# Optimization experiments

Hardware: AMD Instinct MI355X
Metric: run time of the kernel (lower is better)

The kernel has to match this reference:

```python
import jax, jax.numpy as jnp
import numpy as np


def _set_abstraction(xyz, points, npoint, nsample, w1, b1, w2, b2, w3, b3):
    """xyz: (B,3,N), points: (B,C,N) or None. Returns (new_xyz, new_points).
    BN (eval mode) is folded into conv weights/biases; conv1x1 == einsum over channels.
    Deterministic sampling: take first `npoint` points (stand-in for randperm)."""
    B, _, N = xyz.shape
    if npoint is None:
        new_xyz = xyz
        P = N
    else:
        new_xyz = xyz[:, :, :npoint]
        P = npoint
    # squared pairwise distances (B,P,N); topk indices match cdist topk (sqrt monotone)
    xs = jnp.sum(new_xyz * new_xyz, axis=1)            # (B,P)
    ys = jnp.sum(xyz * xyz, axis=1)                    # (B,N)
    d2 = xs[:, :, None] + ys[:, None, :] - 2.0 * jnp.einsum('bcp,bcn->bpn', new_xyz, xyz)
    _, idx = jax.lax.top_k(-d2, nsample)               # (B,P,K) nearest neighbors
    idx4 = idx[:, None, :, :]                          # (B,1,P,K)
    grouped_xyz = jnp.take_along_axis(xyz[:, :, None, :], idx4, axis=3)  # (B,3,P,K)
    grouped_xyz = grouped_xyz - new_xyz[:, :, :, None]
    if points is not None:
        grouped_pts = jnp.take_along_axis(points[:, :, None, :], idx4, axis=3)  # (B,C,P,K)
        feat = jnp.concatenate([grouped_xyz, grouped_pts], axis=1)
    else:
        feat = grouped_xyz
    h = jax.nn.relu(jnp.einsum('oc,bcpk->bopk', w1, feat) + b1[None, :, None, None])
    h = jax.nn.relu(jnp.einsum('oc,bcpk->bopk', w2, h) + b2[None, :, None, None])
    h = jnp.einsum('oc,bcpk->bopk', w3, h) + b3[None, :, None, None]  # no relu before max
    new_points = jnp.max(h, axis=3)                    # (B,C_out,P) max over nsample
    return new_xyz, new_points


def setup_inputs() -> dict:
    key = jax.random.key(0)
    ks = iter(jax.random.split(key, 32))
    B, N, C_IN, NUM_CLASSES = 32, 4096, 6, 40

    def w(k, co, ci):
        return jax.random.normal(k, (co, ci), dtype=jnp.float32) * (1.0 / np.sqrt(ci))

    def b(k, co):
        return jax.random.normal(k, (co,), dtype=jnp.float32) * 0.01

    inp = {'x': jax.random.normal(next(ks), (B, C_IN, N), dtype=jnp.float32)}
    # sa1: in = 3 feat + 3 rel-xyz = 6
    inp['sa1_w1'] = w(next(ks), 64, 6);    inp['sa1_b1'] = b(next(ks), 64)
    inp['sa1_w2'] = w(next(ks), 64, 64);   inp['sa1_b2'] = b(next(ks), 64)
    inp['sa1_w3'] = w(next(ks), 128, 64);  inp['sa1_b3'] = b(next(ks), 128)
    # sa2: in = 128 + 3 = 131
    inp['sa2_w1'] = w(next(ks), 128, 131); inp['sa2_b1'] = b(next(ks), 128)
    inp['sa2_w2'] = w(next(ks), 128, 128); inp['sa2_b2'] = b(next(ks), 128)
    inp['sa2_w3'] = w(next(ks), 256, 128); inp['sa2_b3'] = b(next(ks), 256)
    # sa3: in = 256 + 3 = 259
    inp['sa3_w1'] = w(next(ks), 256, 259); inp['sa3_b1'] = b(next(ks), 256)
    inp['sa3_w2'] = w(next(ks), 512, 256); inp['sa3_b2'] = b(next(ks), 512)
    inp['sa3_w3'] = w(next(ks), 1024, 512); inp['sa3_b3'] = b(next(ks), 1024)
    # fc head (BN folded, dropout in eval mode = identity)
    inp['fc1_w'] = w(next(ks), 512, 1024); inp['fc1_b'] = b(next(ks), 512)
    inp['fc2_w'] = w(next(ks), 256, 512);  inp['fc2_b'] = b(next(ks), 256)
    inp['fc3_w'] = w(next(ks), NUM_CLASSES, 256); inp['fc3_b'] = b(next(ks), NUM_CLASSES)
    return inp


def reference(x, sa1_w1, sa1_b1, sa1_w2, sa1_b2, sa1_w3, sa1_b3,
              sa2_w1, sa2_b1, sa2_w2, sa2_b2, sa2_w3, sa2_b3,
              sa3_w1, sa3_b1, sa3_w2, sa3_b2, sa3_w3, sa3_b3,
              fc1_w, fc1_b, fc2_w, fc2_b, fc3_w, fc3_b):
    xyz = x[:, :3, :]
    pts = x[:, 3:, :]
    xyz1, p1 = _set_abstraction(xyz, pts, 512, 32, sa1_w1, sa1_b1, sa1_w2, sa1_b2, sa1_w3, sa1_b3)
    xyz2, p2 = _set_abstraction(xyz1, p1, 128, 64, sa2_w1, sa2_b1, sa2_w2, sa2_b2, sa2_w3, sa2_b3)
    _, p3 = _set_abstraction(xyz2, p2, None, 1, sa3_w1, sa3_b1, sa3_w2, sa3_b2, sa3_w3, sa3_b3)
    g = jnp.max(p3, axis=2)                               # (B,1024) global max pool
    h = jax.nn.relu(g @ fc1_w.T + fc1_b)                  # dropout eval = identity
    h = jax.nn.relu(h @ fc2_w.T + fc2_b)
    return h @ fc3_w.T + fc3_b                            # (B,num_classes)
```

## Files before the change

kernel.cpp:

```cpp
#include <hip/hip_runtime.h>
#include <hip/hip_bf16.h>

#define FLT_BIG 3.0e38f

typedef __attribute__((ext_vector_type(8))) short s8v;
typedef __attribute__((ext_vector_type(4))) float f4v;

__device__ inline void split2(float v, unsigned short& h0, unsigned short& h1) {
    unsigned int u = __float_as_uint(v);
    unsigned int r0 = (u + 0x7FFFu + ((u >> 16) & 1u)) >> 16;
    h0 = (unsigned short)r0;
    float r = v - __uint_as_float(r0 << 16);
    unsigned int u2 = __float_as_uint(r);
    h1 = (unsigned short)((u2 + 0x7FFFu + ((u2 >> 16) & 1u)) >> 16);
}

#define SA2_P1(AI, BI)                                                          \
    _Pragma("unroll") for (int oi = 0; oi < 2; oi++) {                          \
        _Pragma("unroll") for (int jf = 0; jf < 4; jf++)                        \
            acc1[oi][jf] = __builtin_amdgcn_mfma_f32_16x16x32_bf16(             \
                aw[oi][AI], bfr[jf][BI], acc1[oi][jf], 0, 0, 0);                \
    }
#define SA1_P1(AI, BI)                                                          \
    _Pragma("unroll") for (int jf = 0; jf < 4; jf++)                            \
        acc1[jf] = __builtin_amdgcn_mfma_f32_16x16x32_bf16(                     \
            aw[AI], bfr[jf][BI], acc1[jf], 0, 0, 0);
#define MM_P2(AI, BI)                                                           \
    _Pragma("unroll") for (int oi = 0; oi < 2; oi++) {                          \
        _Pragma("unroll") for (int jf = 0; jf < 4; jf++)                        \
            acc2[oi][jf] = __builtin_amdgcn_mfma_f32_16x16x32_bf16(             \
                af[jf][AI], gw[oi][BI], acc2[oi][jf], 0, 0, 0);                 \
    }
#define SA3_P(AI, BI)                                                           \
    _Pragma("unroll") for (int oi = 0; oi < 2; oi++) {                          \
        _Pragma("unroll") for (int j = 0; j < 4; j++)                           \
            acc[oi][ph * 4 + j] = __builtin_amdgcn_mfma_f32_16x16x32_bf16(      \
                aw[oi][AI], bfh[j][BI], acc[oi][ph * 4 + j], 0, 0, 0);          \
    }

#define MKKEY(QX, QY, QZ, XS)                                                   \
    ({  float dot_ = fmaf((QZ), yz, fmaf((QY), yy, (QX) * yx));                 \
        float d2_ = fmaf(-2.0f, dot_, (XS) + ys);                               \
        unsigned int kk_ = __float_as_uint(d2_);                                \
        (kk_ & 0x80000000u) ? ~kk_ : (kk_ | 0x80000000u); })

struct WfragJob { const float* W; int K, stride, off, no; unsigned short* out; };
struct WfragJobs { WfragJob j[4]; int start[5]; };

__global__ __launch_bounds__(64) void wfrag_multi(WfragJobs jobs) {
    int bid = blockIdx.x;
    int ji = 3;
    if (bid < jobs.start[1]) ji = 0;
    else if (bid < jobs.start[2]) ji = 1;
    else if (bid < jobs.start[3]) ji = 2;
    const WfragJob& J = jobs.j[ji];
    int lb = bid - jobs.start[ji];
    int l = threadIdx.x;
    int ks = lb / J.no, ot = lb - ks * J.no;
    int o = ot * 16 + (l & 15);
    int k0 = ks * 32 + (l >> 4) * 8;
    const float* src = J.W + (size_t)o * J.stride + J.off + k0;
    unsigned short h[2][8];
#pragma unroll
    for (int e = 0; e < 8; e++) split2(src[e], h[0][e], h[1][e]);
#pragma unroll
    for (int p = 0; p < 2; p++) {
        s8v v;
#pragma unroll
        for (int e = 0; e < 8; e++) v[e] = (short)h[p][e];
        *(s8v*)(J.out + ((size_t)(lb * 2 + p) * 64 + l) * 8) = v;
    }
}

#define KNN_CAP 192
__global__ __launch_bounds__(256) void knn4_kernel(
    const float* __restrict__ x, int N_pts, int K, int P,
    int* __restrict__ idx_out, unsigned short* __restrict__ idx16) {
    int bq = blockIdx.x;
    int pg = P >> 2;
    int b = bq / pg, p0 = (bq - b * pg) * 4;
    const float* xyz = x + (size_t)b * 24576;
    __shared__ unsigned int hist[2][2048];
    __shared__ unsigned int candK[4][KNN_CAP];
    __shared__ int candI[4][KNN_CAP];
    __shared__ int outIdx[4][64];
    __shared__ unsigned int cnts[4][2];
    __shared__ int sB[4], sM[4];
    __shared__ float qcoord[4][4];
    int t = threadIdx.x;
    int w = t >> 6, lane = t & 63;
    for (int i = t; i < 4096; i += 256) ((unsigned int*)hist)[i] = 0u;
    if (t < 8) cnts[t >> 1][t & 1] = 0u;
    float qx[4], qy[4], qz[4], xs[4];
#pragma unroll
    for (int q = 0; q < 4; q++) {
        float a = xyz[p0 + q], c1 = xyz[4096 + p0 + q], c2 = xyz[8192 + p0 + q];
        qx[q] = a; qy[q] = c1; qz[q] = c2;
        xs[q] = fmaf(c2, c2, fmaf(c1, c1, a * a));
    }
    if (t < 4) {
        qcoord[t][0] = qx[t]; qcoord[t][1] = qy[t];
        qcoord[t][2] = qz[t]; qcoord[t][3] = xs[t];
    }
    __syncthreads();
    for (int n = t; n < N_pts; n += 256) {
        float yx = xyz[n], yy = xyz[4096 + n], yz = xyz[8192 + n];
        float ys = fmaf(yz, yz, fmaf(yy, yy, yx * yx));
#pragma unroll
        for (int q = 0; q < 4; q++) {
            unsigned int key = MKKEY(qx[q], qy[q], qz[q], xs[q]);
            atomicAdd(&hist[q >> 1][key >> 21], 1u << ((q & 1) * 16));
        }
    }
    __syncthreads();
    {
        int pair = w >> 1, sh = (w & 1) * 16;
        unsigned int lsum = 0;
        for (int i = 0; i < 32; i++)
            lsum += (hist[pair][lane * 32 + i] >> sh) & 0xFFFFu;
        unsigned int incl = lsum;
        for (int ss = 1; ss < 64; ss <<= 1) {
            unsigned int v = (unsigned int)__shfl_up((int)incl, ss);
            if (lane >= ss) incl += v;
        }
        unsigned int excl = incl - lsum;
        if (excl < (unsigned)K && excl + lsum >= (unsigned)K) {
            unsigned int cum = excl;
            for (int i = 0; i < 32; i++) {
                unsigned int h = (hist[pair][lane * 32 + i] >> sh) & 0xFFFFu;
                if (cum < (unsigned)K && cum + h >= (unsigned)K) {
                    sB[w] = lane * 32 + i; sM[w] = (int)cum; break;
                }
                cum += h;
            }
        }
    }
    __syncthreads();
    for (int n = t; n < N_pts; n += 256) {
        float yx = xyz[n], yy = xyz[4096 + n], yz = xyz[8192 + n];
        float ys = fmaf(yz, yz, fmaf(yy, yy, yx * yx));
#pragma unroll
        for (int q = 0; q < 4; q++) {
            unsigned int key = MKKEY(qx[q], qy[q], qz[q], xs[q]);
            int bin = (int)(key >> 21);
            int Bq = sB[q];
            if (bin < Bq) {
                outIdx[q][atomicAdd(&cnts[q][0], 1u)] = n;
            } else if (bin == Bq) {
                unsigned int ci = atomicAdd(&cnts[q][1], 1u);
                if (ci < KNN_CAP) { candK[q][ci] = key; candI[q][ci] = n; }
            }
        }
    }
    __syncthreads();
    {
        int nc = (int)cnts[w][1];
        int m = sM[w], r = K - m, Bw = sB[w];
        if (nc <= KNN_CAP) {
            for (int ci = lane; ci < nc; ci += 64) {
                unsigned int ki = candK[w][ci];
                int ii = candI[w][ci];
                int rank = 0;
                for (int j = 0; j < nc; j++) {
                    unsigned int kj = candK[w][j];
                    rank += (kj < ki || (kj == ki && candI[w][j] < ii)) ? 1 : 0;
                }
                if (rank < r) outIdx[w][m + rank] = ii;
            }
        } else {
            float fqx = qcoord[w][0], fqy = qcoord[w][1];
            float fqz = qcoord[w][2], fxs = qcoord[w][3];
            unsigned int lastK = 0u; int lastI = -1;
            for (int rr = 0; rr < r; rr++) {
                unsigned int bk = 0xFFFFFFFFu; int bi = 0x7fffffff;
                for (int n = lane; n < N_pts; n += 64) {
                    float yx = xyz[n], yy = xyz[4096 + n], yz = xyz[8192 + n];
                    float ys = fmaf(yz, yz, fmaf(yy, yy, yx * yx));
                    unsigned int key = MKKEY(fqx, fqy, fqz, fxs);
                    if ((int)(key >> 21) == Bw) {
                        bool gt = (key > lastK) || (key == lastK && n > lastI);
                        if (gt && (key < bk || (key == bk && n < bi))) { bk = key; bi = n; }
                    }
                }
#pragma unroll
                for (int ss = 32; ss > 0; ss >>= 1) {
                    unsigned int ok = (unsigned int)__shfl_xor((int)bk, ss);
                    int oi = __shfl_xor(bi, ss);
                    if (ok < bk || (ok == bk && oi < bi)) { bk = ok; bi = oi; }
                }
                if (lane == 0) outIdx[w][m + rr] = bi;
                lastK = bk; lastI = bi;
            }
        }
    }
    __syncthreads();
    if (t < 4 * K) {
        int q = t / K, k = t - q * K;
        size_t off = ((size_t)(b * P) + p0 + q) * K + k;
        if (idx16) idx16[off] = (unsigned short)outIdx[q][k];
        else idx_out[off] = outIdx[q][k];
    }
}

__global__ __launch_bounds__(256) void sa1_pre_kernel(
    const float* __restrict__ x, const float* __restrict__ w1, const float* __restrict__ b1,
    float* __restrict__ a1t) {
    int bid = blockIdx.x;
    int b = bid >> 5, nt = bid & 31, n0 = nt << 7;
    __shared__ float xsh[6 * 128];
    __shared__ float wt[6 * 68];
    const float* xb = x + (size_t)b * 24576;
    int t = threadIdx.x;
    for (int id = t; id < 768; id += 256) {
        int c = id >> 7, n = id & 127;
        xsh[c * 128 + n] = xb[c * 4096 + n0 + n];
    }
    for (int id = t; id < 384; id += 256) {
        int c = id >> 6, o = id & 63;
        wt[c * 68 + o] = w1[o * 6 + c];
    }
    __syncthreads();
    int o = t & 63, ng = t >> 6;
    float acc[32];
    float bias = b1[o];
#pragma unroll
    for (int j = 0; j < 32; j++) acc[j] = bias;
    for (int c = 0; c < 6; c++) {
        float w = wt[c * 68 + o];
        const float* f = &xsh[c * 128 + ng * 32];
#pragma unroll
        for (int j = 0; j < 32; j++) acc[j] += w * f[j];
    }
#pragma unroll
    for (int j = 0; j < 32; j++)
        a1t[((size_t)b * 4096 + n0 + ng * 32 + j) * 64 + o] = acc[j];
}

__global__ __launch_bounds__(256) void sa1_mfma_kernel(
    const float* __restrict__ x, const float* __restrict__ a1t,
    const int* __restrict__ idx1, const float* __restrict__ w1,
    const unsigned short* __restrict__ w2f, const float* __restrict__ b2,
    const unsigned short* __restrict__ w3f, const float* __restrict__ b3,
    float* __restrict__ p1) {
    int bp = blockIdx.x;
    int b = bp >> 8, pp = bp & 255, p0 = pp * 2;
    __shared__ float dshq[2][64];
    __shared__ int nbr[64];
    __shared__ unsigned short A1buf[8 * 2 * 64 * 8];
    __shared__ float MX[2][128];
    const float* xb = x + (size_t)b * 24576;
    int t = threadIdx.x;
    int w = t >> 6, l = t & 63;
    int n16 = l & 15, og = l >> 4;
    if (t < 64) nbr[t] = idx1[((size_t)b * 512 + p0) * 32 + t];
    if (t < 128) {
        int qi = t >> 6, c = t & 63;
        float qx = xb[p0 + qi], qy = xb[4096 + p0 + qi], qz = xb[8192 + p0 + qi];
        dshq[qi][c] = -(w1[c * 6 + 0] * qx + w1[c * 6 + 1] * qy + w1[c * 6 + 2] * qz);
    }
    __syncthreads();
    int q = w >> 1;
    f4v acc1[4];
#pragma unroll
    for (int jf = 0; jf < 4; jf++) acc1[jf] = (f4v){0.f, 0.f, 0.f, 0.f};
    const float* gsrc = a1t + ((size_t)b * 4096 + nbr[w * 16 + n16]) * 64 + og * 8;
    f4v nv0 = *(const f4v*)(gsrc);
    f4v nv1 = *(const f4v*)(gsrc + 4);
    s8v nw[2];
    {
        const s8v* wr = (const s8v*)w2f;
#pragma unroll
        for (int pl = 0; pl < 2; pl++) nw[pl] = wr[(w * 2 + pl) * 64 + l];
    }
    for (int ks = 0; ks < 2; ks++) {
        f4v v0 = nv0, v1 = nv1;
        s8v aw[2];
#pragma unroll
        for (int pl = 0; pl < 2; pl++) aw[pl] = nw[pl];
        if (ks < 1) {
            nv0 = *(const f4v*)(gsrc + 32);
            nv1 = *(const f4v*)(gsrc + 36);
            const s8v* wr = (const s8v*)w2f + (size_t)4 * 2 * 64;
#pragma unroll
            for (int pl = 0; pl < 2; pl++) nw[pl] = wr[(w * 2 + pl) * 64 + l];
        }
        unsigned short* BFD = A1buf + (ks & 1) * 4096;
        const float* d = &dshq[q][ks * 32 + og * 8];
        s8v sp0, sp1;
#pragma unroll
        for (int e = 0; e < 8; e++) {
            float hv = fmaxf(((e < 4) ? v0[e] : v1[e - 4]) + d[e], 0.f);
            unsigned short h0, h1;
            split2(hv, h0, h1);
            sp0[e] = (short)h0; sp1[e] = (short)h1;
        }
        *(s8v*)&BFD[((w * 2 + 0) * 64 + l) * 8] = sp0;
        *(s8v*)&BFD[((w * 2 + 1) * 64 + l) * 8] = sp1;
        __syncthreads();
        s8v bfr[4][2];
#pragma unroll
        for (int jf = 0; jf < 4; jf++)
#pragma unroll
            for (int pl = 0; pl < 2; pl++)
                bfr[jf][pl] = *(const s8v*)&BFD[((jf * 2 + pl) * 64 + l) * 8];
        SA1_P1(1, 0) SA1_P1(0, 1) SA1_P1(0, 0)
    }
    __syncthreads();
    {
        f4v bv = *(const f4v*)(b2 + w * 16 + og * 4);
        int l2 = n16 + ((w & 1) * 2 + (og >> 1)) * 16;
        int half = og & 1;
#pragma unroll
        for (int jf = 0; jf < 4; jf++) {
            unsigned short hh[2][4];
#pragma unroll
            for (int r = 0; r < 4; r++) {
                float y = fmaxf(acc1[jf][r] + bv[r], 0.f);
                split2(y, hh[0][r], hh[1][r]);
            }
            int slot = (w >> 1) * 4 + jf;
#pragma unroll
            for (int pl = 0; pl < 2; pl++) {
                unsigned long long pk = (unsigned long long)hh[pl][0] |
                    ((unsigned long long)hh[pl][1] << 16) |
                    ((unsigned long long)hh[pl][2] << 32) |
                    ((unsigned long long)hh[pl][3] << 48);
                *(unsigned long long*)&A1buf[((slot * 2 + pl) * 64 + l2) * 8 + half * 4] = pk;
            }
        }
    }
    __syncthreads();
    f4v acc2[2][4];
#pragma unroll
    for (int oi = 0; oi < 2; oi++)
#pragma unroll
        for (int jf = 0; jf < 4; jf++) acc2[oi][jf] = (f4v){0.f, 0.f, 0.f, 0.f};
    for (int ks2 = 0; ks2 < 2; ks2++) {
        s8v af[4][2];
#pragma unroll
        for (int jf = 0; jf < 4; jf++)
#pragma unroll
            for (int pl = 0; pl < 2; pl++)
                af[jf][pl] = *(const s8v*)&A1buf[(((ks2 * 4 + jf) * 2 + pl) * 64 + l) * 8];
        const s8v* wr = (const s8v*)w3f + (size_t)(ks2 * 8) * 2 * 64;
        s8v gw[2][2];
#pragma unroll
        for (int oi = 0; oi < 2; oi++)
#pragma unroll
            for (int pl = 0; pl < 2; pl++)
                gw[oi][pl] = wr[((w * 2 + oi) * 2 + pl) * 64 + l];
        MM_P2(1, 0) MM_P2(0, 1) MM_P2(0, 0)
    }
#pragma unroll
    for (int oi = 0; oi < 2; oi++) {
        float m0 = fmaxf(fmaxf(acc2[oi][0][0], acc2[oi][0][1]),
                         fmaxf(acc2[oi][0][2], acc2[oi][0][3]));
        m0 = fmaxf(m0, fmaxf(fmaxf(acc2[oi][1][0], acc2[oi][1][1]),
                             fmaxf(acc2[oi][1][2], acc2[oi][1][3])));
        float m1 = fmaxf(fmaxf(acc2[oi][2][0], acc2[oi][2][1]),
                         fmaxf(acc2[oi][2][2], acc2[oi][2][3]));
        m1 = fmaxf(m1, fmaxf(fmaxf(acc2[oi][3][0], acc2[oi][3][1]),
                             fmaxf(acc2[oi][3][2], acc2[oi][3][3])));
        m0 = fmaxf(m0, __shfl_xor(m0, 16));
        m0 = fmaxf(m0, __shfl_xor(m0, 32));
        m1 = fmaxf(m1, __shfl_xor(m1, 16));
        m1 = fmaxf(m1, __shfl_xor(m1, 32));
        if (og == 0) {
            MX[0][(w * 2 + oi) * 16 + n16] = m0;
            MX[1][(w * 2 + oi) * 16 + n16] = m1;
        }
    }
    __syncthreads();
    {
        int o = t & 127, qq = t >> 7;
        p1[((size_t)b * 128 + o) * 512 + p0 + qq] = MX[qq][o] + b3[o];
    }
}

__global__ __launch_bounds__(256) void sa2_pre_kernel(
    const float* __restrict__ x, const float* __restrict__ p1,
    const float* __restrict__ w1, const float* __restrict__ b1,
    float* __restrict__ a2t) {
    int bid = blockIdx.x;
    int b = bid >> 2, nt = bid & 3, n0 = nt << 7;
    __shared__ float ins[2][16 * 128];
    __shared__ float wt[2][16 * 132];
    const float* xb = x + (size_t)b * 24576;
    const float* p1b = p1 + (size_t)b * 65536;
    int t = threadIdx.x;
    int og = t >> 3, pg = t & 7;
    int o0 = og * 4;
    float acc[4][16];
    {
        float bl[4] = {b1[o0], b1[o0 + 1], b1[o0 + 2], b1[o0 + 3]};
#pragma unroll
        for (int oi = 0; oi < 4; oi++)
#pragma unroll
            for (int j = 0; j < 16; j++) acc[oi][j] = bl[oi];
    }
    for (int id = t; id < 16 * 128; id += 256) {
        int n = id & 127, c = id >> 7;
        ins[0][c * 128 + n] = (c < 3) ? xb[c * 4096 + n0 + n]
                                      : p1b[(size_t)(c - 3) * 512 + n0 + n];
    }
    for (int id = t; id < 2048; id += 256) {
        int c = id & 15, oo = id >> 4;
        wt[0][c * 132 + oo] = w1[oo * 131 + c];
    }
    __syncthreads();
    for (int ch = 0; ch < 9; ch++) {
        int cs = (ch == 8) ? 3 : 16;
        if (ch < 8) {
            int c0n = (ch + 1) * 16;
            int csn = (ch == 7) ? 3 : 16;
            int nb = (ch + 1) & 1;
            for (int id = t; id < csn * 128; id += 256) {
                int n = id & 127, c = id >> 7;
                int cg = c0n + c;
                ins[nb][c * 128 + n] = (cg < 3) ? xb[cg * 4096 + n0 + n]
                                                : p1b[(size_t)(cg - 3) * 512 + n0 + n];
            }
            for (int id = t; id < 2048; id += 256) {
                int c = id & 15, oo = id >> 4;
                if (c < csn) wt[nb][c * 132 + oo] = w1[oo * 131 + c0n + c];
            }
        }
        const float* wb = wt[ch & 1];
        const float* ib = ins[ch & 1];
        for (int cc = 0; cc < cs; cc++) {
            float4 wv = *(const float4*)&wb[cc * 132 + o0];
            float wl[4] = {wv.x, wv.y, wv.z, wv.w};
#pragma unroll
            for (int c4 = 0; c4 < 4; c4++) {
                float4 fv = *(const float4*)&ib[cc * 128 + pg * 4 + c4 * 32];
                float fl[4] = {fv.x, fv.y, fv.z, fv.w};
#pragma unroll
                for (int j = 0; j < 4; j++)
#pragma unroll
                    for (int oi = 0; oi < 4; oi++) acc[oi][c4 * 4 + j] += wl[oi] * fl[j];
            }
        }
        __syncthreads();
    }
#pragma unroll
    for (int c4 = 0; c4 < 4; c4++)
#pragma unroll
        for (int j = 0; j < 4; j++) {
            int n = n0 + pg * 4 + c4 * 32 + j;
            float4 v;
            v.x = acc[0][c4 * 4 + j]; v.y = acc[1][c4 * 4 + j];
            v.z = acc[2][c4 * 4 + j]; v.w = acc[3][c4 * 4 + j];
            *(float4*)&a2t[((size_t)b * 512 + n) * 128 + o0] = v;
        }
}

__global__ __launch_bounds__(256) void sa2_mfma_kernel(
    const float* __restrict__ x, const float* __restrict__ a2t,
    const unsigned short* __restrict__ idx2, const float* __restrict__ w1,
    const unsigned short* __restrict__ w2f, const float* __restrict__ b2,
    const unsigned short* __restrict__ w3f, const float* __restrict__ b3,
    unsigned short* __restrict__ p2f) {
    int bp = blockIdx.x;
    int b = bp >> 7, p = bp & 127;
    __shared__ float dsh[128];
    __shared__ int nbr[64];
    __shared__ unsigned short A2buf[16 * 2 * 64 * 8];
    __shared__ float MX[256];
    const float* xb = x + (size_t)b * 24576;
    int t = threadIdx.x;
    int w = t >> 6, l = t & 63;
    int n16 = l & 15, og = l >> 4;
    if (t < 64) nbr[t] = (int)idx2[((size_t)b * 128 + p) * 64 + t];
    if (t < 128) {
        float qx = xb[p], qy = xb[4096 + p], qz = xb[8192 + p];
        dsh[t] = -(w1[t * 131 + 0] * qx + w1[t * 131 + 1] * qy + w1[t * 131 + 2] * qz);
    }
    __syncthreads();
    f4v acc1[2][4];
#pragma unroll
    for (int oi = 0; oi < 2; oi++)
#pragma unroll
        for (int jf = 0; jf < 4; jf++) acc1[oi][jf] = (f4v){0.f, 0.f, 0.f, 0.f};
    const float* gsrc = a2t + ((size_t)b * 512 + nbr[w * 16 + n16]) * 128 + og * 8;
    f4v nv0 = *(const f4v*)(gsrc);
    f4v nv1 = *(const f4v*)(gsrc + 4);
    s8v nw[2][2];
    {
        const s8v* wr = (const s8v*)w2f;
#pragma unroll
        for (int oi = 0; oi < 2; oi++)
#pragma unroll
            for (int pl = 0; pl < 2; pl++)
                nw[oi][pl] = wr[((w * 2 + oi) * 2 + pl) * 64 + l];
    }
    for (int ks = 0; ks < 4; ks++) {
        f4v v0 = nv0, v1 = nv1;
        s8v aw[2][2];
#pragma unroll
        for (int oi = 0; oi < 2; oi++)
#pragma unroll
            for (int pl = 0; pl < 2; pl++) aw[oi][pl] = nw[oi][pl];
        if (ks < 3) {
            nv0 = *(const f4v*)(gsrc + (ks + 1) * 32);
            nv1 = *(const f4v*)(gsrc + (ks + 1) * 32 + 4);
            const s8v* wr = (const s8v*)w2f + (size_t)((ks + 1) * 8) * 2 * 64;
#pragma unroll
            for (int oi = 0; oi < 2; oi++)
#pragma unroll
                for (int pl = 0; pl < 2; pl++)
                    nw[oi][pl] = wr[((w * 2 + oi) * 2 + pl) * 64 + l];
        }
        unsigned short* BFD = A2buf + (ks & 1) * 4096;
        const float* d = &dsh[ks * 32 + og * 8];
        s8v sp0, sp1;
#pragma unroll
        for (int e = 0; e < 8; e++) {
            float hv = fmaxf(((e < 4) ? v0[e] : v1[e - 4]) + d[e], 0.f);
            unsigned short h0, h1;
            split2(hv, h0, h1);
            sp0[e] = (short)h0; sp1[e] = (short)h1;
        }
        *(s8v*)&BFD[((w * 2 + 0) * 64 + l) * 8] = sp0;
        *(s8v*)&BFD[((w * 2 + 1) * 64 + l) * 8] = sp1;
        __syncthreads();
        s8v bfr[4][2];
#pragma unroll
        for (int jf = 0; jf < 4; jf++)
#pragma unroll
            for (int pl = 0; pl < 2; pl++)
                bfr[jf][pl] = *(const s8v*)&BFD[((jf * 2 + pl) * 64 + l) * 8];
        SA2_P1(1, 0) SA2_P1(0, 1) SA2_P1(0, 0)
    }
    __syncthreads();
#pragma unroll
    for (int oi = 0; oi < 2; oi++) {
        int ot = w * 2 + oi;
        f4v bv = *(const f4v*)(b2 + ot * 16 + og * 4);
        int l2 = n16 + (oi * 2 + (og >> 1)) * 16;
        int half = og & 1;
#pragma unroll
        for (int jf = 0; jf < 4; jf++) {
            unsigned short hh[2][4];
#pragma unroll
            for (int r = 0; r < 4; r++) {
                float y = fmaxf(acc1[oi][jf][r] + bv[r], 0.f);
                split2(y, hh[0][r], hh[1][r]);
            }
            int slot = w * 4 + jf;
#pragma unroll
            for (int pl = 0; pl < 2; pl++) {
                unsigned long long pk = (unsigned long long)hh[pl][0] |
                    ((unsigned long long)hh[pl][1] << 16) |
                    ((unsigned long long)hh[pl][2] << 32) |
                    ((unsigned long long)hh[pl][3] << 48);
                *(unsigned long long*)&A2buf[((slot * 2 + pl) * 64 + l2) * 8 + half * 4] = pk;
            }
        }
    }
    __syncthreads();
#pragma unroll
    for (int half2 = 0; half2 < 2; half2++) {
        f4v acc2[2][4];
#pragma unroll
        for (int oi = 0; oi < 2; oi++)
#pragma unroll
            for (int jf = 0; jf < 4; jf++) acc2[oi][jf] = (f4v){0.f, 0.f, 0.f, 0.f};
        for (int ks2 = 0; ks2 < 4; ks2++) {
            s8v af[4][2];
#pragma unroll
            for (int jf = 0; jf < 4; jf++)
#pragma unroll
                for (int pl = 0; pl < 2; pl++)
                    af[jf][pl] = *(const s8v*)&A2buf[(((ks2 * 4 + jf) * 2 + pl) * 64 + l) * 8];
            const s8v* wr = (const s8v*)w3f + (size_t)(ks2 * 16) * 2 * 64;
            s8v gw[2][2];
#pragma unroll
            for (int oi = 0; oi < 2; oi++)
#pragma unroll
                for (int pl = 0; pl < 2; pl++)
                    gw[oi][pl] = wr[((w * 4 + half2 * 2 + oi) * 2 + pl) * 64 + l];
            MM_P2(1, 0) MM_P2(0, 1) MM_P2(0, 0)
        }
#pragma unroll
        for (int oi = 0; oi < 2; oi++) {
            float m = -FLT_BIG;
#pragma unroll
            for (int jf = 0; jf < 4; jf++) {
                float mj = fmaxf(fmaxf(acc2[oi][jf][0], acc2[oi][jf][1]),
                                 fmaxf(acc2[oi][jf][2], acc2[oi][jf][3]));
                m = fmaxf(m, mj);
            }
            m = fmaxf(m, __shfl_xor(m, 16));
            m = fmaxf(m, __shfl_xor(m, 32));
            if (og == 0) MX[(w * 4 + half2 * 2 + oi) * 16 + n16] = m;
        }
    }
    __syncthreads();
    {
        float val = MX[t] + b3[t];
        unsigned short h0, h1;
        split2(val, h0, h1);
        int pt = p >> 4;
        int ks = t >> 5, kl = t & 31;
        int l2 = (p & 15) + (kl >> 3) * 16;
        int e = kl & 7;
        size_t fb = (((size_t)b * 64 + ks * 8 + pt) * 2) * 512 + l2 * 8 + e;
        p2f[fb] = h0;
        p2f[fb + 512] = h1;
    }
}

__global__ __launch_bounds__(64) void sa3_mfma_kernel(
    const unsigned short* __restrict__ hf_in, const unsigned short* __restrict__ wf,
    const float* __restrict__ bias, int nks, int noCout,
    unsigned short* __restrict__ hf_out, int nksOut,
    float* __restrict__ gout, int reduce) {
    int nb = noCout >> 1;
    int bid = blockIdx.x;
    int b = bid / nb, u = bid - b * nb;
    int ot0 = u * 2;
    int l = threadIdx.x;
    f4v acc[2][8];
#pragma unroll
    for (int oi = 0; oi < 2; oi++)
#pragma unroll
        for (int j = 0; j < 8; j++) acc[oi][j] = (f4v){0.f, 0.f, 0.f, 0.f};
    const unsigned short* hb = hf_in + (size_t)b * nks * 8 * 2 * 512;
    for (int ks = 0; ks < nks; ks++) {
        s8v aw[2][2];
#pragma unroll
        for (int oi = 0; oi < 2; oi++)
#pragma unroll
            for (int pl = 0; pl < 2; pl++)
                aw[oi][pl] = *(const s8v*)&wf[(((size_t)(ks * noCout + ot0 + oi)) * 2 + pl) * 512 + l * 8];
#pragma unroll
        for (int ph = 0; ph < 2; ph++) {
            s8v bfh[4][2];
#pragma unroll
            for (int j = 0; j < 4; j++)
#pragma unroll
                for (int pl = 0; pl < 2; pl++)
                    bfh[j][pl] = *(const s8v*)&hb[(((size_t)(ks * 8 + ph * 4 + j)) * 2 + pl) * 512 + l * 8];
            SA3_P(1, 0) SA3_P(0, 1) SA3_P(0, 0)
        }
    }
    if (!reduce) {
#pragma unroll
        for (int oi = 0; oi < 2; oi++) {
            int OT = ot0 + oi;
            f4v bv = *(const f4v*)(bias + OT * 16 + (l >> 4) * 4);
            int ksp = OT >> 1;
            int l2 = (l & 15) + ((OT & 1) * 2 + ((l >> 4) >> 1)) * 16;
            int base4 = ((l >> 4) & 1) * 4;
#pragma unroll
            for (int pt = 0; pt < 8; pt++) {
                unsigned short hh[2][4];
#pragma unroll
                for (int r = 0; r < 4; r++) {
                    float y = fmaxf(acc[oi][pt][r] + bv[r], 0.f);
                    split2(y, hh[0][r], hh[1][r]);
                }
#pragma unroll
                for (int pl = 0; pl < 2; pl++) {
                    unsigned long long pk = (unsigned long long)hh[pl][0] |
                        ((unsigned long long)hh[pl][1] << 16) |
                        ((unsigned long long)hh[pl][2] << 32) |
                        ((unsigned long long)hh[pl][3] << 48);
                    *(unsigned long long*)&hf_out[
                        (((size_t)b * nksOut * 8 + ksp * 8 + pt) * 2 + pl) * 512 + l2 * 8 + base4] = pk;
                }
            }
        }
    } else {
        int Cout = noCout * 16;
#pragma unroll
        for (int oi = 0; oi < 2; oi++) {
            int OT = ot0 + oi;
#pragma unroll
            for (int r = 0; r < 4; r++) {
                float m = acc[oi][0][r];
#pragma unroll
                for (int pt = 1; pt < 8; pt++) m = fmaxf(m, acc[oi][pt][r]);
                m = fmaxf(m, __shfl_xor(m, 1));
                m = fmaxf(m, __shfl_xor(m, 2));
                m = fmaxf(m, __shfl_xor(m, 4));
                m = fmaxf(m, __shfl_xor(m, 8));
                if ((l & 15) == 0) {
                    int o = OT * 16 + ((l >> 4) << 2) + r;
                    gout[(size_t)b * Cout + o] = m + bias[o];
                }
            }
        }
    }
}

__global__ __launch_bounds__(256) void head1_kernel(
    const float* __restrict__ g, const float* __restrict__ fw1,
    const float* __restrict__ fb1, float* __restrict__ h1out) {
    int bid = blockIdx.x;
    int b = bid >> 3, u = bid & 7;
    int o0 = u * 64;
    __shared__ float gs[1024];
    int t = threadIdx.x;
    for (int i = t; i < 1024; i += 256) gs[i] = g[(size_t)b * 1024 + i];
    __syncthreads();
    int o = o0 + (t >> 2), seg = t & 3;
    const float4* wr = (const float4*)&fw1[(size_t)o * 1024 + seg * 256];
    const float* gg0 = &gs[seg * 256];
    float acc = 0.f;
    for (int c = 0; c < 64; c++) {
        float4 wv = wr[c];
        const float* gg = &gg0[c * 4];
        acc += wv.x * gg[0] + wv.y * gg[1] + wv.z * gg[2] + wv.w * gg[3];
    }
    acc += __shfl_down(acc, 1);
    acc += __shfl_down(acc, 2);
    if (seg == 0) h1out[(size_t)b * 512 + o] = fmaxf(acc + fb1[o], 0.f);
}

__global__ __launch_bounds__(256) void head2_kernel(
    const float* __restrict__ h1in,
    const float* __restrict__ fw2, const float* __restrict__ fb2,
    const float* __restrict__ fw3, const float* __restrict__ fb3,
    float* __restrict__ out) {
    int b = blockIdx.x;
    int t = threadIdx.x;
    __shared__ float h1[512];
    __shared__ float h2[256];
    for (int i = t; i < 512; i += 256) h1[i] = h1in[(size_t)b * 512 + i];
    __syncthreads();
    {
        float acc = fb2[t];
        const float4* wr = (const float4*)&fw2[(size_t)t * 512];
        for (int c = 0; c < 128; c++) {
            float4 wv = wr[c];
            acc += wv.x * h1[c * 4] + wv.y * h1[c * 4 + 1] + wv.z * h1[c * 4 + 2] + wv.w * h1[c * 4 + 3];
        }
        h2[t] = fmaxf(acc, 0.f);
    }
    __syncthreads();
    if (t < 40) {
        float acc = fb3[t];
        const float4* wr = (const float4*)&fw3[(size_t)t * 256];
        for (int c = 0; c < 64; c++) {
            float4 wv = wr[c];
            acc += wv.x * h2[c * 4] + wv.y * h2[c * 4 + 1] + wv.z * h2[c * 4 + 2] + wv.w * h2[c * 4 + 3];
        }
        out[b * 40 + t] = acc;
    }
}

extern "C" void kernel_launch(void* const* d_in, const int* in_sizes, int n_in,
                              void* d_out, int out_size, void* d_ws, size_t ws_size,
                              hipStream_t stream) {
    const float* x      = (const float*)d_in[0];
    const float* sa1_w1 = (const float*)d_in[1];
    const float* sa1_b1 = (const float*)d_in[2];
    const float* sa1_w2 = (const float*)d_in[3];
    const float* sa1_b2 = (const float*)d_in[4];
    const float* sa1_w3 = (const float*)d_in[5];
    const float* sa1_b3 = (const float*)d_in[6];
    const float* sa2_w1 = (const float*)d_in[7];
    const float* sa2_b1 = (const float*)d_in[8];
    const float* sa2_w2 = (const float*)d_in[9];
    const float* sa2_b2 = (const float*)d_in[10];
    const float* sa2_w3 = (const float*)d_in[11];
    const float* sa2_b3 = (const float*)d_in[12];
    const float* sa3_w1 = (const float*)d_in[13];
    const float* sa3_b1 = (const float*)d_in[14];
    const float* sa3_w2 = (const float*)d_in[15];
    const float* sa3_b2 = (const float*)d_in[16];
    const float* sa3_w3 = (const float*)d_in[17];
    const float* sa3_b3 = (const float*)d_in[18];
    const float* fc1_w  = (const float*)d_in[19];
    const float* fc1_b  = (const float*)d_in[20];
    const float* fc2_w  = (const float*)d_in[21];
    const float* fc2_b  = (const float*)d_in[22];
    const float* fc3_w  = (const float*)d_in[23];
    const float* fc3_b  = (const float*)d_in[24];

    char* ws = (char*)d_ws;
    const size_t MB = 1048576;
    const size_t KB = 1024;
    unsigned short* s1w2f = (unsigned short*)(ws + 0);
    unsigned short* s1w3f = (unsigned short*)(ws + 32 * KB);
    unsigned short* s2w2f = (unsigned short*)(ws + 128 * KB);
    unsigned short* s2w3f = (unsigned short*)(ws + 224 * KB);
    int*            idx1  = (int*)(ws + 512 * KB);
    unsigned short* idx2  = (unsigned short*)(ws + 2560 * KB);
    float*          a1t   = (float*)(ws + 3 * MB);
    float*          p1    = (float*)(ws + 35 * MB);
    float*          a2t   = (float*)(ws + 4 * MB);
    unsigned short* p2f   = (unsigned short*)(ws + 12 * MB);
    unsigned short* h1f   = (unsigned short*)(ws + 18 * MB);
    unsigned short* h2f   = (unsigned short*)(ws + 24 * MB);
    float*          g     = (float*)(ws + 36 * MB);
    float*          h1hd  = (float*)(ws + 36 * MB + 128 * KB);
    unsigned short* w1f3  = (unsigned short*)(ws + 36 * MB + 512 * KB);
    unsigned short* w2f3  = (unsigned short*)(ws + 37 * MB);
    unsigned short* w3f3  = (unsigned short*)(ws + 38 * MB);

    {
        WfragJobs jobs;
        jobs.j[0] = {sa1_w2, 64, 64, 0, 4, s1w2f};
        jobs.j[1] = {sa1_w3, 64, 64, 0, 8, s1w3f};
        jobs.j[2] = {sa2_w2, 128, 128, 0, 8, s2w2f};
        jobs.j[3] = {sa2_w3, 128, 128, 0, 16, s2w3f};
        jobs.start[0] = 0; jobs.start[1] = 8; jobs.start[2] = 24;
        jobs.start[3] = 56; jobs.start[4] = 120;
        wfrag_multi<<<120, 64, 0, stream>>>(jobs);
    }
    knn4_kernel<<<32 * 128, 256, 0, stream>>>(x, 4096, 32, 512, idx1, nullptr);
    sa1_pre_kernel<<<32 * 32, 256, 0, stream>>>(x, sa1_w1, sa1_b1, a1t);
    sa1_mfma_kernel<<<32 * 256, 256, 0, stream>>>(x, a1t, idx1, sa1_w1,
                                                  s1w2f, sa1_b2, s1w3f, sa1_b3, p1);
    knn4_kernel<<<32 * 32, 256, 0, stream>>>(x, 512, 64, 128, nullptr, idx2);
    sa2_pre_kernel<<<32 * 4, 256, 0, stream>>>(x, p1, sa2_w1, sa2_b1, a2t);
    {
        WfragJobs jobs;
        jobs.j[0] = {sa3_w1, 256, 259, 3, 16, w1f3};
        jobs.j[1] = {sa3_w2, 256, 256, 0, 32, w2f3};
        jobs.j[2] = {sa3_w3, 512, 512, 0, 64, w3f3};
        jobs.j[3] = {sa3_w3, 512, 512, 0, 64, w3f3};
        jobs.start[0] = 0; jobs.start[1] = 128; jobs.start[2] = 384;
        jobs.start[3] = 1408; jobs.start[4] = 1408;
        wfrag_multi<<<1408, 64, 0, stream>>>(jobs);
    }
    sa2_mfma_kernel<<<32 * 128, 256, 0, stream>>>(x, a2t, idx2, sa2_w1,
                                                  s2w2f, sa2_b2, s2w3f, sa2_b3, p2f);
    sa3_mfma_kernel<<<32 * 8, 64, 0, stream>>>(p2f, w1f3, sa3_b1, 8, 16, h1f, 8, nullptr, 0);
    sa3_mfma_kernel<<<32 * 16, 64, 0, stream>>>(h1f, w2f3, sa3_b2, 8, 32, h2f, 16, nullptr, 0);
    sa3_mfma_kernel<<<32 * 32, 64, 0, stream>>>(h2f, w3f3, sa3_b3, 16, 64, nullptr, 0, g, 1);
    head1_kernel<<<32 * 8, 256, 0, stream>>>(g, fc1_w, fc1_b, h1hd);
    head2_kernel<<<32, 256, 0, stream>>>(h1hd, fc2_w, fc2_b, fc3_w, fc3_b,
                                         (float*)d_out);
}
```

Baseline: 397.4 us.

## Cache 16-bit distance keys in LDS and process two queries per KNN block

The KNN kernel now handles two query points per block instead of four, doubling the grid. It stores the top 16 bits of each point's key for both queries in shared memory during the histogram pass. The second pass then reads those cached keys instead of reloading coordinates and recomputing distances. Only candidates in the boundary bin recompute the full key, and the candidate capacity rises to 256. In exchange, half the waves in each block sit idle during the selection phases, and per-block LDS use grows.

After: 425.7 us. +7.1%, slower.

```diff
diff --git a/kernel.cpp b/kernel.cpp
--- a/kernel.cpp
+++ b/kernel.cpp
@@ -72,33 +72,34 @@
     }
 }
 
-#define KNN_CAP 192
-__global__ __launch_bounds__(256) void knn4_kernel(
+#define KNN_CAP 256
+__global__ __launch_bounds__(256) void knn2q_kernel(
     const float* __restrict__ x, int N_pts, int K, int P,
     int* __restrict__ idx_out, unsigned short* __restrict__ idx16) {
     int bq = blockIdx.x;
-    int pg = P >> 2;
-    int b = bq / pg, p0 = (bq - b * pg) * 4;
+    int pg = P >> 1;
+    int b = bq / pg, p0 = (bq - b * pg) * 2;
     const float* xyz = x + (size_t)b * 24576;
-    __shared__ unsigned int hist[2][2048];
-    __shared__ unsigned int candK[4][KNN_CAP];
-    __shared__ int candI[4][KNN_CAP];
-    __shared__ int outIdx[4][64];
-    __shared__ unsigned int cnts[4][2];
-    __shared__ int sB[4], sM[4];
-    __shared__ float qcoord[4][4];
+    __shared__ unsigned int hist[2048];
+    __shared__ unsigned int keys16[4096];
+    __shared__ unsigned int candK[2][KNN_CAP];
+    __shared__ int candI[2][KNN_CAP];
+    __shared__ int outIdx[2][64];
+    __shared__ unsigned int cnts[2][2];
+    __shared__ int sB[2], sM[2];
+    __shared__ float qcoord[2][4];
     int t = threadIdx.x;
     int w = t >> 6, lane = t & 63;
-    for (int i = t; i < 4096; i += 256) ((unsigned int*)hist)[i] = 0u;
-    if (t < 8) cnts[t >> 1][t & 1] = 0u;
-    float qx[4], qy[4], qz[4], xs[4];
-#pragma unroll
-    for (int q = 0; q < 4; q++) {
+    for (int i = t; i < 2048; i += 256) hist[i] = 0u;
+    if (t < 4) cnts[t >> 1][t & 1] = 0u;
+    float qx[2], qy[2], qz[2], xs[2];
+#pragma unroll
+    for (int q = 0; q < 2; q++) {
         float a = xyz[p0 + q], c1 = xyz[4096 + p0 + q], c2 = xyz[8192 + p0 + q];
         qx[q] = a; qy[q] = c1; qz[q] = c2;
         xs[q] = fmaf(c2, c2, fmaf(c1, c1, a * a));
     }
-    if (t < 4) {
+    if (t < 2) {
         qcoord[t][0] = qx[t]; qcoord[t][1] = qy[t];
         qcoord[t][2] = qz[t]; qcoord[t][3] = xs[t];
     }
@@ -106,18 +107,18 @@
     for (int n = t; n < N_pts; n += 256) {
         float yx = xyz[n], yy = xyz[4096 + n], yz = xyz[8192 + n];
         float ys = fmaf(yz, yz, fmaf(yy, yy, yx * yx));
-#pragma unroll
-        for (int q = 0; q < 4; q++) {
-            unsigned int key = MKKEY(qx[q], qy[q], qz[q], xs[q]);
-            atomicAdd(&hist[q >> 1][key >> 21], 1u << ((q & 1) * 16));
-        }
-    }
-    __syncthreads();
-    {
-        int pair = w >> 1, sh = (w & 1) * 16;
+        unsigned int k0 = MKKEY(qx[0], qy[0], qz[0], xs[0]);
+        unsigned int k1 = MKKEY(qx[1], qy[1], qz[1], xs[1]);
+        atomicAdd(&hist[k0 >> 21], 1u);
+        atomicAdd(&hist[k1 >> 21], 0x10000u);
+        keys16[n] = (k0 >> 16) | ((k1 >> 16) << 16);
+    }
+    __syncthreads();
+    if (w < 2) {
+        int sh = w * 16;
         unsigned int lsum = 0;
         for (int i = 0; i < 32; i++)
-            lsum += (hist[pair][lane * 32 + i] >> sh) & 0xFFFFu;
+            lsum += (hist[lane * 32 + i] >> sh) & 0xFFFFu;
         unsigned int incl = lsum;
         for (int ss = 1; ss < 64; ss <<= 1) {
             unsigned int v = (unsigned int)__shfl_up((int)incl, ss);
@@ -127,7 +128,7 @@
         if (excl < (unsigned)K && excl + lsum >= (unsigned)K) {
             unsigned int cum = excl;
             for (int i = 0; i < 32; i++) {
-                unsigned int h = (hist[pair][lane * 32 + i] >> sh) & 0xFFFFu;
+                unsigned int h = (hist[lane * 32 + i] >> sh) & 0xFFFFu;
                 if (cum < (unsigned)K && cum + h >= (unsigned)K) {
                     sB[w] = lane * 32 + i; sM[w] = (int)cum; break;
                 }
@@ -137,23 +138,27 @@
     }
     __syncthreads();
     for (int n = t; n < N_pts; n += 256) {
-        float yx = xyz[n], yy = xyz[4096 + n], yz = xyz[8192 + n];
-        float ys = fmaf(yz, yz, fmaf(yy, yy, yx * yx));
-#pragma unroll
-        for (int q = 0; q < 4; q++) {
-            unsigned int key = MKKEY(qx[q], qy[q], qz[q], xs[q]);
-            int bin = (int)(key >> 21);
+        unsigned int kk = keys16[n];
+#pragma unroll
+        for (int q = 0; q < 2; q++) {
+            unsigned int k16 = (kk >> (q * 16)) & 0xFFFFu;
+            int bin = (int)(k16 >> 5);
             int Bq = sB[q];
             if (bin < Bq) {
                 outIdx[q][atomicAdd(&cnts[q][0], 1u)] = n;
             } else if (bin == Bq) {
                 unsigned int ci = atomicAdd(&cnts[q][1], 1u);
-                if (ci < KNN_CAP) { candK[q][ci] = key; candI[q][ci] = n; }
-            }
-        }
-    }
-    __syncthreads();
-    {
+                if (ci < KNN_CAP) {
+                    float yx = xyz[n], yy = xyz[4096 + n], yz = xyz[8192 + n];
+                    float ys = fmaf(yz, yz, fmaf(yy, yy, yx * yx));
+                    unsigned int key = MKKEY(qx[q], qy[q], qz[q], xs[q]);
+                    candK[q][ci] = key; candI[q][ci] = n;
+                }
+            }
+        }
+    }
+    __syncthreads();
+    if (w < 2) {
         int nc = (int)cnts[w][1];
         int m = sM[w], r = K - m, Bw = sB[w];
         if (nc <= KNN_CAP) {
@@ -194,7 +199,7 @@
         }
     }
     __syncthreads();
-    if (t < 4 * K) {
+    if (t < 2 * K) {
         int q = t / K, k = t - q * K;
         size_t off = ((size_t)(b * P) + p0 + q) * K + k;
         if (idx16) idx16[off] = (unsigned short)outIdx[q][k];
@@ -810,11 +815,11 @@
         jobs.start[3] = 56; jobs.start[4] = 120;
         wfrag_multi<<<120, 64, 0, stream>>>(jobs);
     }
-    knn4_kernel<<<32 * 128, 256, 0, stream>>>(x, 4096, 32, 512, idx1, nullptr);
+    knn2q_kernel<<<32 * 256, 256, 0, stream>>>(x, 4096, 32, 512, idx1, nullptr);
     sa1_pre_kernel<<<32 * 32, 256, 0, stream>>>(x, sa1_w1, sa1_b1, a1t);
     sa1_mfma_kernel<<<32 * 256, 256, 0, stream>>>(x, a1t, idx1, sa1_w1,
                                                   s1w2f, sa1_b2, s1w3f, sa1_b3, p1);
-    knn4_kernel<<<32 * 32, 256, 0, stream>>>(x, 512, 64, 128, nullptr, idx2);
+    knn2q_kernel<<<32 * 64, 256, 0, stream>>>(x, 512, 64, 128, nullptr, idx2);
     sa2_pre_kernel<<<32 * 4, 256, 0, stream>>>(x, p1, sa2_w1, sa2_b1, a2t);
     {
         WfragJobs jobs;
```
